# Kernel tuning notes

Hardware: AMD Instinct MI355X
Metric: run time of the kernel (lower is better)

## Reference

```python
import jax, jax.numpy as jnp
import numpy as np

HEADS = 2
BN_EPS = 1e-5


def _upsample2x_bilinear_ac(x):
    # torch nn.Upsample(scale_factor=2, mode='bilinear', align_corners=True)
    B, C, H, W = x.shape

    def grid(n):
        c = jnp.arange(2 * n) * ((n - 1) / (2 * n - 1))  # align_corners mapping
        i0 = jnp.clip(jnp.floor(c).astype(jnp.int32), 0, n - 2)
        w = (c - i0).astype(x.dtype)
        return i0, w

    i0, wh = grid(H)
    j0, ww = grid(W)
    x = x[:, :, i0, :] * (1 - wh)[None, None, :, None] + x[:, :, i0 + 1, :] * wh[None, None, :, None]
    x = x[:, :, :, j0] * (1 - ww) + x[:, :, :, j0 + 1] * ww
    return x


def _self_attn(x, wq, wkv, wo, wob):
    # x: (b, t, d); lucidrains axial_attention SelfAttention
    b, t, d = x.shape
    e = d // HEADS
    q = x @ wq
    k, v = jnp.split(x @ wkv, 2, axis=-1)
    mh = lambda z: z.reshape(b, t, HEADS, e).transpose(0, 2, 1, 3)  # (b,h,t,e)
    q, k, v = mh(q), mh(k), mh(v)
    dots = jnp.einsum('bhie,bhje->bhij', q, k) * (e ** -0.5)
    attn = jax.nn.softmax(dots, axis=-1)
    o = jnp.einsum('bhij,bhje->bhie', attn, v)
    o = o.transpose(0, 2, 1, 3).reshape(b, t, d)
    return o @ wo + wob


def setup_inputs() -> dict:
    key = jax.random.key(0)
    ks = jax.random.split(key, 16)
    C, E = 256, 128
    cat = 2 * C + E
    s = 0.02
    inp = {
        'x': jax.random.normal(ks[0], (4, C, 64, 64), jnp.float32),
        'res': jax.random.normal(ks[1], (4, E, 128, 128), jnp.float32),
        'wq_h': jax.random.normal(ks[2], (C, C), jnp.float32) * s,
        'wkv_h': jax.random.normal(ks[3], (C, 2 * C), jnp.float32) * s,
        'wo_h': jax.random.normal(ks[4], (C, C), jnp.float32) * s,
        'wob_h': jnp.zeros((C,), jnp.float32),
        'wq_w': jax.random.normal(ks[5], (C, C), jnp.float32) * s,
        'wkv_w': jax.random.normal(ks[6], (C, 2 * C), jnp.float32) * s,
        'wo_w': jax.random.normal(ks[7], (C, C), jnp.float32) * s,
        'wob_w': jnp.zeros((C,), jnp.float32),
        'conv_w': jax.random.normal(ks[8], (cat, E), jnp.float32) * s,
        'gamma': jnp.ones((E,), jnp.float32),
        'beta': jnp.zeros((E,), jnp.float32),
    }
    return inp


def reference(x, res, wq_h, wkv_h, wo_h, wob_h, wq_w, wkv_w, wo_w, wob_w, conv_w, gamma, beta):
    xu = _upsample2x_bilinear_ac(x)  # (B,C,2H,2W)
    B, C, H, W = xu.shape
    # axial attention along H (rows): batch over B*W
    ah = xu.transpose(0, 3, 2, 1).reshape(B * W, H, C)
    ah = _self_attn(ah, wq_h, wkv_h, wo_h, wob_h).reshape(B, W, H, C).transpose(0, 3, 2, 1)
    # axial attention along W (cols): batch over B*H
    aw = xu.transpose(0, 2, 3, 1).reshape(B * H, W, C)
    aw = _self_attn(aw, wq_w, wkv_w, wo_w, wob_w).reshape(B, H, W, C).transpose(0, 3, 1, 2)
    x_attn = jax.nn.relu(ah + aw)  # sum_axial_out=True, then ReLU
    cat = jnp.concatenate([x_attn, xu, res], axis=1)  # (B, 2C+E, H, W)
    y = jnp.einsum('bchw,ce->behw', cat, conv_w)  # conv1x1, no bias
    y = jax.nn.relu(y)
    # BatchNorm2d, training-mode batch stats (biased variance)
    mu = y.mean(axis=(0, 2, 3), keepdims=True)
    var = y.var(axis=(0, 2, 3), keepdims=True)
    y = (y - mu) / jnp.sqrt(var + BN_EPS)
    return y * gamma[None, :, None, None] + beta[None, :, None, None]
```

## Files before the change

### kernel.cpp

```cpp
#include <hip/hip_runtime.h>
#include <hip/hip_bf16.h>
#include <cstdio>


typedef short bf16x8 __attribute__((ext_vector_type(8)));
typedef short bf16x4 __attribute__((ext_vector_type(4)));
typedef float f32x4 __attribute__((ext_vector_type(4)));

#define MFMA16(a, b, c) __builtin_amdgcn_mfma_f32_16x16x32_bf16((a), (b), (c), 0, 0, 0)

__device__ __forceinline__ short f2bf(float v) {
  __hip_bfloat16 h = __float2bfloat16(v);
  union { __hip_bfloat16 h; short s; } u; u.h = h; return u.s;
}
__device__ __forceinline__ float bf2f(short s) {
  return __uint_as_float(((unsigned int)(unsigned short)s) << 16);
}
__device__ __forceinline__ int swz(int row, int col) {
  return col ^ ((row & 7) << 3);
}

struct WtAll {
  const float* src[7];
  short* dst[7];
  int K[7], N[7], tile0[7];
};

__global__ __launch_bounds__(256) void k_wt_all(WtAll P) {
  const int bid = blockIdx.x;
  int i = 0;
#pragma unroll
  for (int j = 1; j < 7; j++) if (bid >= P.tile0[j]) i = j;
  const float* src = P.src[i];
  short* dst = P.dst[i];
  const int K = P.K[i], N = P.N[i];
  const int local = bid - P.tile0[i];
  const int ktiles = K >> 5;
  const int nt = local / ktiles, kt = local - nt * ktiles;
  const int k0 = kt * 32, n0 = nt * 32;
  __shared__ float tile[32][33];
  const int tx = threadIdx.x & 31, ty = threadIdx.x >> 5;
#pragma unroll
  for (int r = 0; r < 4; r++)
    tile[ty + r * 8][tx] = src[(size_t)(k0 + ty + r * 8) * N + n0 + tx];
  __syncthreads();
#pragma unroll
  for (int r = 0; r < 4; r++)
    dst[(size_t)(n0 + ty + r * 8) * K + k0 + tx] = f2bf(tile[tx][ty + r * 8]);
}

__global__ __launch_bounds__(256) void k_upsample(const float* __restrict__ x,
                                                  short* __restrict__ xu) {
  __shared__ float ldsV[64][65];
  const int bh = blockIdx.x, z = blockIdx.y;
  const int b = bh >> 7, h = bh & 127;
  const float chf = h * (63.0f / 127.0f);
  int i0 = (int)chf; if (i0 > 62) i0 = 62;
  const float wh = chf - (float)i0;
  const int t = threadIdx.x;
  const int cbase = z * 64;
  const float* xb = x + ((size_t)(b * 256 + cbase) * 64 + i0) * 64;
#pragma unroll
  for (int p = 0; p < 16; p++) {
    const int li = p * 256 + t;
    const int c = li >> 6, w = li & 63;
    const float* px = xb + (size_t)c * 4096 + w;
    const float v0 = px[0], v1 = px[64];
    ldsV[c][w] = v0 * (1.f - wh) + v1 * wh;
  }
  __syncthreads();
  const int cg = t & 7, wi = t >> 3;
  short* xout = xu + (size_t)(bh * 128) * 256 + cbase + cg * 8;
#pragma unroll
  for (int p = 0; p < 4; p++) {
    const int w = p * 32 + wi;
    const float cwf = w * (63.0f / 127.0f);
    int j0 = (int)cwf; if (j0 > 62) j0 = 62;
    const float ww = cwf - (float)j0;
    bf16x8 o;
#pragma unroll
    for (int u = 0; u < 8; u++) {
      const float v0 = ldsV[cg * 8 + u][j0], v1 = ldsV[cg * 8 + u][j0 + 1];
      o[u] = f2bf(v0 * (1.f - ww) + v1 * ww);
    }
    *(bf16x8*)(xout + (size_t)w * 256) = o;
  }
}

__global__ __launch_bounds__(512, 2) void k_fused(const short* __restrict__ xu,
                                                  const short* __restrict__ wqkvT0,
                                                  const short* __restrict__ woT0,
                                                  const float* __restrict__ wob0,
                                                  const float* __restrict__ wob1,
                                                  short* __restrict__ accb0,
                                                  short* __restrict__ accb1) {
  __shared__ __align__(16) short Xs[128][256];
  __shared__ __align__(16) short Qb[128][128];
  __shared__ __align__(16) short Kb[128][128];
  __shared__ __align__(16) short Vtb[128][128];

  const int dir = blockIdx.y;
  const short* wqkvT = wqkvT0 + (size_t)dir * 196608;
  const short* woT   = woT0 + (size_t)dir * 65536;
  const float* wob   = dir ? wob1 : wob0;
  short* accb        = dir ? accb1 : accb0;

  const int s = blockIdx.x;
  const int b = s >> 7, pos = s & 127;
  const int tok0 = b * 16384 + (dir ? pos * 128 : pos);
  const int tstep = dir ? 1 : 128;
  const int tid = threadIdx.x;
  const int lane = tid & 63, wid = tid >> 6;
  const int lr = lane & 15, kb = lane >> 4;
  const int ct = wid * 16;
  const float scale = 0.08838834764831845f;

#pragma unroll
  for (int p = 0; p < 8; p++) {
    const int u = p * 512 + tid;
    const int row = u >> 5, ck = (u & 31) * 8;
    bf16x8 v = *(const bf16x8*)(xu + (size_t)(tok0 + row * tstep) * 256 + ck);
    *(bf16x8*)&Xs[row][swz(row, ck)] = v;
  }

  f32x4 accp[2][8];
#pragma unroll
  for (int i = 0; i < 2; i++)
#pragma unroll
    for (int j = 0; j < 8; j++) accp[i][j] = (f32x4){0.f, 0.f, 0.f, 0.f};

  for (int h = 0; h < 2; h++) {
    const short* wqb = wqkvT + (size_t)(h * 128 + ct + lr) * 256 + kb * 8;
    const short* wkb = wqkvT + (size_t)(256 + h * 128 + ct + lr) * 256 + kb * 8;
    const short* wvb = wqkvT + (size_t)(512 + h * 128 + ct + lr) * 256 + kb * 8;
    bf16x8 wq[8], wk[8], wv[8];
#pragma unroll
    for (int ks = 0; ks < 8; ks++) {
      wq[ks] = *(const bf16x8*)(wqb + ks * 32);
      wk[ks] = *(const bf16x8*)(wkb + ks * 32);
      wv[ks] = *(const bf16x8*)(wvb + ks * 32);
    }

    __syncthreads();

#pragma unroll
    for (int nt = 0; nt < 8; nt++) {
      const int xrow = nt * 16 + lr;
      f32x4 dq = (f32x4){0.f, 0.f, 0.f, 0.f};
      f32x4 dk = (f32x4){0.f, 0.f, 0.f, 0.f};
      f32x4 dv = (f32x4){0.f, 0.f, 0.f, 0.f};
#pragma unroll
      for (int ks = 0; ks < 8; ks++) {
        bf16x8 xf = *(const bf16x8*)&Xs[xrow][swz(xrow, kb * 8 + ks * 32)];
        dq = MFMA16(wq[ks], xf, dq);
        dk = MFMA16(wk[ks], xf, dk);
        dv = MFMA16(xf, wv[ks], dv);
      }
      const int trow = nt * 16 + lr, cc = ct + kb * 4;
      bf16x4 pq = {f2bf(dq[0]), f2bf(dq[1]), f2bf(dq[2]), f2bf(dq[3])};
      bf16x4 pk = {f2bf(dk[0]), f2bf(dk[1]), f2bf(dk[2]), f2bf(dk[3])};
      *(bf16x4*)&Qb[trow][swz(trow, cc)] = pq;
      *(bf16x4*)&Kb[trow][swz(trow, cc)] = pk;
      const int vrow = ct + lr;
      bf16x4 pv = {f2bf(dv[0]), f2bf(dv[1]), f2bf(dv[2]), f2bf(dv[3])};
      *(bf16x4*)&Vtb[vrow][swz(vrow, nt * 16 + kb * 4)] = pv;
    }

    __syncthreads();

    f32x4 s8[8];
#pragma unroll
    for (int i = 0; i < 8; i++) s8[i] = (f32x4){0.f, 0.f, 0.f, 0.f};
    const int qrow = ct + lr;
#pragma unroll
    for (int ks = 0; ks < 4; ks++) {
      bf16x8 aq = *(const bf16x8*)&Qb[qrow][swz(qrow, kb * 8 + ks * 32)];
#pragma unroll
      for (int nj = 0; nj < 8; nj++) {
        const int krow = nj * 16 + lr;
        bf16x8 bk = *(const bf16x8*)&Kb[krow][swz(krow, kb * 8 + ks * 32)];
        s8[nj] = MFMA16(bk, aq, s8[nj]);
      }
    }
    {
      float m = s8[0][0];
#pragma unroll
      for (int nj = 0; nj < 8; nj++)
#pragma unroll
        for (int r = 0; r < 4; r++) m = fmaxf(m, s8[nj][r]);
      m = fmaxf(m, __shfl_xor(m, 16));
      m = fmaxf(m, __shfl_xor(m, 32));
      float sum = 0.f;
#pragma unroll
      for (int nj = 0; nj < 8; nj++)
#pragma unroll
        for (int r = 0; r < 4; r++) {
          s8[nj][r] = __expf((s8[nj][r] - m) * scale);
          sum += s8[nj][r];
        }
      sum += __shfl_xor(sum, 16);
      sum += __shfl_xor(sum, 32);
      const float inv = 1.f / sum;
#pragma unroll
      for (int nj = 0; nj < 8; nj++) {
        bf16x4 pp = {f2bf(s8[nj][0] * inv), f2bf(s8[nj][1] * inv),
                     f2bf(s8[nj][2] * inv), f2bf(s8[nj][3] * inv)};
        *(bf16x4*)&Qb[qrow][swz(qrow, nj * 16 + kb * 4)] = pp;
      }
    }

    f32x4 o8[8];
#pragma unroll
    for (int i = 0; i < 8; i++) o8[i] = (f32x4){0.f, 0.f, 0.f, 0.f};
#pragma unroll
    for (int ks = 0; ks < 4; ks++) {
      bf16x8 bp = *(const bf16x8*)&Qb[qrow][swz(qrow, kb * 8 + ks * 32)];
#pragma unroll
      for (int mi = 0; mi < 8; mi++) {
        const int vrow = mi * 16 + lr;
        bf16x8 av = *(const bf16x8*)&Vtb[vrow][swz(vrow, kb * 8 + ks * 32)];
        o8[mi] = MFMA16(av, bp, o8[mi]);
      }
    }

    __syncthreads();

#pragma unroll
    for (int mi = 0; mi < 8; mi++) {
      const int cc = mi * 16 + kb * 4;
      bf16x4 po = {f2bf(o8[mi][0]), f2bf(o8[mi][1]), f2bf(o8[mi][2]), f2bf(o8[mi][3])};
      *(bf16x4*)&Kb[qrow][swz(qrow, cc)] = po;
    }

    __syncthreads();

    {
      const short* w0 = woT + (size_t)(wid * 32 + lr) * 256 + h * 128 + kb * 8;
      const short* w1 = woT + (size_t)(wid * 32 + 16 + lr) * 256 + h * 128 + kb * 8;
      bf16x8 wa[4], wb2[4];
#pragma unroll
      for (int ks = 0; ks < 4; ks++) {
        wa[ks]  = *(const bf16x8*)(w0 + ks * 32);
        wb2[ks] = *(const bf16x8*)(w1 + ks * 32);
      }
#pragma unroll
      for (int nt = 0; nt < 8; nt++) {
        const int trow = nt * 16 + lr;
#pragma unroll
        for (int ks = 0; ks < 4; ks++) {
          bf16x8 bo = *(const bf16x8*)&Kb[trow][swz(trow, kb * 8 + ks * 32)];
          accp[0][nt] = MFMA16(wa[ks], bo, accp[0][nt]);
          accp[1][nt] = MFMA16(wb2[ks], bo, accp[1][nt]);
        }
      }
    }
  }

#pragma unroll
  for (int mi2 = 0; mi2 < 2; mi2++) {
    const int outc = wid * 32 + mi2 * 16 + kb * 4;
    const float b0 = wob[outc], b1 = wob[outc + 1];
    const float b2 = wob[outc + 2], b3 = wob[outc + 3];
#pragma unroll
    for (int nt = 0; nt < 8; nt++) {
      const int token = tok0 + (nt * 16 + lr) * tstep;
      bf16x4 pv = {f2bf(accp[mi2][nt][0] + b0), f2bf(accp[mi2][nt][1] + b1),
                   f2bf(accp[mi2][nt][2] + b2), f2bf(accp[mi2][nt][3] + b3)};
      *(bf16x4*)(accb + (size_t)token * 256 + outc) = pv;
    }
  }
}

__global__ __launch_bounds__(256) void k_gemm_conv(const short* __restrict__ accb0,
                                                   const short* __restrict__ accb1,
                                                   const short* __restrict__ xu,
                                                   const float* __restrict__ res,
                                                   const short* __restrict__ Bt,
                                                   float* __restrict__ ytmp,
                                                   float* __restrict__ partial) {
  __shared__ float redS[2][128], redS2[2][128];
  const int tid = threadIdx.x;
  const int lane = tid & 63, wid = tid >> 6;
  const int lr = lane & 15, kb = lane >> 4;
  const int wr = wid >> 1, wc = wid & 1;
  const int m0 = blockIdx.y * 128;
  f32x4 acc[4][4];
#pragma unroll
  for (int i = 0; i < 4; i++)
#pragma unroll
    for (int j = 0; j < 4; j++) acc[i][j] = (f32x4){0.f, 0.f, 0.f, 0.f};
  const short* arow0 = accb0 + (size_t)(m0 + wr * 64 + lr) * 256 + kb * 8;
  const short* arow1 = accb1 + (size_t)(m0 + wr * 64 + lr) * 256 + kb * 8;
  const short* arow2 = xu + (size_t)(m0 + wr * 64 + lr) * 256 + kb * 8;
  const short* brow = Bt + (size_t)(wc * 64 + lr) * 640 + kb * 8;
#pragma unroll
  for (int ks = 0; ks < 8; ks++) {
    bf16x8 a[4], b[4];
#pragma unroll
    for (int mi = 0; mi < 4; mi++) {
      bf16x8 t0 = *(const bf16x8*)(arow0 + (size_t)mi * 16 * 256 + ks * 32);
      bf16x8 t1 = *(const bf16x8*)(arow1 + (size_t)mi * 16 * 256 + ks * 32);
      bf16x8 tv;
#pragma unroll
      for (int u = 0; u < 8; u++) {
        float sv = bf2f(t0[u]) + bf2f(t1[u]);
        tv[u] = f2bf(fmaxf(sv, 0.f));
      }
      a[mi] = tv;
    }
#pragma unroll
    for (int nj = 0; nj < 4; nj++)
      b[nj] = *(const bf16x8*)(brow + (size_t)nj * 16 * 640 + ks * 32);
#pragma unroll
    for (int mi = 0; mi < 4; mi++)
#pragma unroll
      for (int nj = 0; nj < 4; nj++)
        acc[mi][nj] = MFMA16(a[mi], b[nj], acc[mi][nj]);
  }
#pragma unroll
  for (int ks = 8; ks < 16; ks++) {
    bf16x8 a[4], b[4];
#pragma unroll
    for (int mi = 0; mi < 4; mi++)
      a[mi] = *(const bf16x8*)(arow2 + (size_t)mi * 16 * 256 + (ks - 8) * 32);
#pragma unroll
    for (int nj = 0; nj < 4; nj++)
      b[nj] = *(const bf16x8*)(brow + (size_t)nj * 16 * 640 + ks * 32);
#pragma unroll
    for (int mi = 0; mi < 4; mi++)
#pragma unroll
      for (int nj = 0; nj < 4; nj++)
        acc[mi][nj] = MFMA16(a[mi], b[nj], acc[mi][nj]);
  }
  const int bC = (m0 >> 14) * 128;
  const int hh = (m0 >> 7) & 127;
#pragma unroll
  for (int ks = 16; ks < 20; ks++) {
    const int e0 = (ks - 16) * 32 + kb * 8;
    bf16x8 a[4], b[4];
#pragma unroll
    for (int mi = 0; mi < 4; mi++) {
      const int wl = wr * 64 + mi * 16 + lr;
      const float* rp = res + ((size_t)(bC + e0) * 128 + hh) * 128 + wl;
      bf16x8 tv;
#pragma unroll
      for (int u = 0; u < 8; u++) tv[u] = f2bf(rp[(size_t)u * 16384]);
      a[mi] = tv;
    }
#pragma unroll
    for (int nj = 0; nj < 4; nj++)
      b[nj] = *(const bf16x8*)(brow + (size_t)nj * 16 * 640 + ks * 32);
#pragma unroll
    for (int mi = 0; mi < 4; mi++)
#pragma unroll
      for (int nj = 0; nj < 4; nj++)
        acc[mi][nj] = MFMA16(a[mi], b[nj], acc[mi][nj]);
  }
#pragma unroll
  for (int nj = 0; nj < 4; nj++) {
    float s = 0.f, s2 = 0.f;
    const int c = wc * 64 + nj * 16 + lr;
#pragma unroll
    for (int mi = 0; mi < 4; mi++) {
      const int rbase = m0 + wr * 64 + mi * 16 + kb * 4;
#pragma unroll
      for (int r = 0; r < 4; r++) {
        const float yv = fmaxf(acc[mi][nj][r], 0.f);
        ytmp[(size_t)(rbase + r) * 128 + c] = yv;
        s += yv; s2 += yv * yv;
      }
    }
    s += __shfl_xor(s, 16);  s += __shfl_xor(s, 32);
    s2 += __shfl_xor(s2, 16); s2 += __shfl_xor(s2, 32);
    if (kb == 0) { redS[wr][c] = s; redS2[wr][c] = s2; }
  }
  __syncthreads();
  if (tid < 128) {
    partial[((size_t)blockIdx.y * 128 + tid) * 2]     = redS[0][tid] + redS[1][tid];
    partial[((size_t)blockIdx.y * 128 + tid) * 2 + 1] = redS2[0][tid] + redS2[1][tid];
  }
}

__global__ __launch_bounds__(128) void k_bnstats2(const float* __restrict__ partial,
                                                  float* __restrict__ stats) {
  const int ch = threadIdx.x;
  float s = 0.f, s2 = 0.f;
  for (int i = 0; i < 512; i++) {
    s  += partial[(size_t)(i * 128 + ch) * 2];
    s2 += partial[(size_t)(i * 128 + ch) * 2 + 1];
  }
  const float mu = s * (1.f / 65536.f);
  const float var = s2 * (1.f / 65536.f) - mu * mu;
  stats[ch * 2] = mu;
  stats[ch * 2 + 1] = rsqrtf(var + 1e-5f);
}

__global__ __launch_bounds__(256) void k_bnout(const float* __restrict__ y,
                                               const float* __restrict__ stats,
                                               const float* __restrict__ gamma,
                                               const float* __restrict__ beta,
                                               float* __restrict__ out) {
  const int bh = blockIdx.x;
  const int b = bh >> 7, h = bh & 127;
  const int w = threadIdx.x & 127, half = threadIdx.x >> 7;
  const float* yp = y + (size_t)(bh * 128 + w) * 128 + half * 64;
  float* op = out + ((size_t)(b * 128) << 14) + h * 128 + w;
#pragma unroll
  for (int e4 = 0; e4 < 16; e4++) {
    f32x4 v = *(const f32x4*)(yp + e4 * 4);
#pragma unroll
    for (int u = 0; u < 4; u++) {
      const int e = half * 64 + e4 * 4 + u;
      const float mu = stats[e * 2], rstd = stats[e * 2 + 1];
      op[(size_t)e << 14] = (v[u] - mu) * rstd * gamma[e] + beta[e];
    }
  }
}

extern "C" void kernel_launch(void* const* d_in, const int* in_sizes, int n_in,
                              void* d_out, int out_size, void* d_ws, size_t ws_size,
                              hipStream_t stream) {
  const float* x      = (const float*)d_in[0];
  const float* res    = (const float*)d_in[1];
  const float* wq_h   = (const float*)d_in[2];
  const float* wkv_h  = (const float*)d_in[3];
  const float* wo_h   = (const float*)d_in[4];
  const float* wob_h  = (const float*)d_in[5];
  const float* wq_w   = (const float*)d_in[6];
  const float* wkv_w  = (const float*)d_in[7];
  const float* wo_w   = (const float*)d_in[8];
  const float* wob_w  = (const float*)d_in[9];
  const float* conv_w = (const float*)d_in[10];
  const float* gamma  = (const float*)d_in[11];
  const float* beta   = (const float*)d_in[12];

  char* ws = (char*)d_ws;
  short* wqkvT[2] = {(short*)(ws + 0), (short*)(ws + 393216)};
  short* woT[2]   = {(short*)(ws + 786432), (short*)(ws + 917504)};
  short* convT    = (short*)(ws + 1048576);
  short* xu       = (short*)(ws + 1245184);
  float* ytmp     = (float*)(ws + 34799616);
  float* partial  = (float*)(ws + 68354048);
  float* stats    = (float*)(ws + 68878336);
  short* accb1    = (short*)(ws + 68879360);
  short* accb0    = (short*)d_out;
  float* out      = (float*)d_out;

  if (ws_size < 102433792ull)
    fprintf(stderr, "kernel_launch: ws_size %zu too small\n", ws_size);

  WtAll P;
  P.src[0] = wq_h;  P.dst[0] = wqkvT[0];          P.K[0] = 256; P.N[0] = 256; P.tile0[0] = 0;
  P.src[1] = wkv_h; P.dst[1] = wqkvT[0] + 65536;  P.K[1] = 256; P.N[1] = 512; P.tile0[1] = 64;
  P.src[2] = wq_w;  P.dst[2] = wqkvT[1];          P.K[2] = 256; P.N[2] = 256; P.tile0[2] = 192;
  P.src[3] = wkv_w; P.dst[3] = wqkvT[1] + 65536;  P.K[3] = 256; P.N[3] = 512; P.tile0[3] = 256;
  P.src[4] = wo_h;  P.dst[4] = woT[0];            P.K[4] = 256; P.N[4] = 256; P.tile0[4] = 384;
  P.src[5] = wo_w;  P.dst[5] = woT[1];            P.K[5] = 256; P.N[5] = 256; P.tile0[5] = 448;
  P.src[6] = conv_w;P.dst[6] = convT;             P.K[6] = 640; P.N[6] = 128; P.tile0[6] = 512;
  k_wt_all<<<592, 256, 0, stream>>>(P);

  k_upsample<<<dim3(512, 4), 256, 0, stream>>>(x, xu);

  k_fused<<<dim3(512, 2), 512, 0, stream>>>(xu, wqkvT[0], woT[0],
                                            wob_h, wob_w, accb0, accb1);

  k_gemm_conv<<<dim3(1, 512), 256, 0, stream>>>(accb0, accb1, xu, res, convT,
                                                ytmp, partial);
  k_bnstats2<<<1, 128, 0, stream>>>(partial, stats);
  k_bnout<<<512, 256, 0, stream>>>(ytmp, stats, gamma, beta, out);
}
```

Measured before the change: 247.9 us.

## Write transposed upsample copy and stream X from global to shrink fused-kernel LDS

The upsample kernel now also writes a W-major transposed copy of the upsampled tensor, so both attention directions read contiguous rows. The fused attention kernel drops its X and V shared-memory tiles, reading X fragments directly from global/L2 and reusing the K buffer for V and the Q buffer for the attention output. Launch bounds rise from 2 to 4 blocks per CU to exploit the smaller LDS footprint. This trades extra global writes and repeated global reads of X, plus extra barriers, for higher occupancy; register pressure under the tighter bound may cause spills.

```diff
diff --git a/kernel.cpp b/kernel.cpp
--- a/kernel.cpp
+++ b/kernel.cpp
@@ -50,7 +50,8 @@
 }
 
 __global__ __launch_bounds__(256) void k_upsample(const float* __restrict__ x,
-                                                  short* __restrict__ xu) {
+                                                  short* __restrict__ xu,
+                                                  short* __restrict__ xuT) {
   __shared__ float ldsV[64][65];
   const int bh = blockIdx.x, z = blockIdx.y;
   const int b = bh >> 7, h = bh & 127;
@@ -71,6 +72,7 @@
   __syncthreads();
   const int cg = t & 7, wi = t >> 3;
   short* xout = xu + (size_t)(bh * 128) * 256 + cbase + cg * 8;
+  short* xoutT = xuT + ((size_t)b * 16384 + h) * 256 + cbase + cg * 8;
 #pragma unroll
   for (int p = 0; p < 4; p++) {
     const int w = p * 32 + wi;
@@ -84,20 +86,20 @@
       o[u] = f2bf(v0 * (1.f - ww) + v1 * ww);
     }
     *(bf16x8*)(xout + (size_t)w * 256) = o;
-  }
-}
-
-__global__ __launch_bounds__(512, 2) void k_fused(const short* __restrict__ xu,
+    *(bf16x8*)(xoutT + (size_t)w * 128 * 256) = o;
+  }
+}
+
+__global__ __launch_bounds__(512, 4) void k_fused(const short* __restrict__ xu,
+                                                  const short* __restrict__ xuT,
                                                   const short* __restrict__ wqkvT0,
                                                   const short* __restrict__ woT0,
                                                   const float* __restrict__ wob0,
                                                   const float* __restrict__ wob1,
                                                   short* __restrict__ accb0,
                                                   short* __restrict__ accb1) {
-  __shared__ __align__(16) short Xs[128][256];
   __shared__ __align__(16) short Qb[128][128];
   __shared__ __align__(16) short Kb[128][128];
-  __shared__ __align__(16) short Vtb[128][128];
 
   const int dir = blockIdx.y;
   const short* wqkvT = wqkvT0 + (size_t)dir * 196608;
@@ -109,20 +111,14 @@
   const int b = s >> 7, pos = s & 127;
   const int tok0 = b * 16384 + (dir ? pos * 128 : pos);
   const int tstep = dir ? 1 : 128;
+  const short* Xb = (dir ? xu : xuT) + ((size_t)b * 16384 + (size_t)pos * 128) * 256;
+
   const int tid = threadIdx.x;
   const int lane = tid & 63, wid = tid >> 6;
   const int lr = lane & 15, kb = lane >> 4;
   const int ct = wid * 16;
   const float scale = 0.08838834764831845f;
 
-#pragma unroll
-  for (int p = 0; p < 8; p++) {
-    const int u = p * 512 + tid;
-    const int row = u >> 5, ck = (u & 31) * 8;
-    bf16x8 v = *(const bf16x8*)(xu + (size_t)(tok0 + row * tstep) * 256 + ck);
-    *(bf16x8*)&Xs[row][swz(row, ck)] = v;
-  }
-
   f32x4 accp[2][8];
 #pragma unroll
   for (int i = 0; i < 2; i++)
@@ -130,42 +126,33 @@
     for (int j = 0; j < 8; j++) accp[i][j] = (f32x4){0.f, 0.f, 0.f, 0.f};
 
   for (int h = 0; h < 2; h++) {
-    const short* wqb = wqkvT + (size_t)(h * 128 + ct + lr) * 256 + kb * 8;
-    const short* wkb = wqkvT + (size_t)(256 + h * 128 + ct + lr) * 256 + kb * 8;
-    const short* wvb = wqkvT + (size_t)(512 + h * 128 + ct + lr) * 256 + kb * 8;
-    bf16x8 wq[8], wk[8], wv[8];
-#pragma unroll
-    for (int ks = 0; ks < 8; ks++) {
-      wq[ks] = *(const bf16x8*)(wqb + ks * 32);
-      wk[ks] = *(const bf16x8*)(wkb + ks * 32);
-      wv[ks] = *(const bf16x8*)(wvb + ks * 32);
-    }
-
-    __syncthreads();
-
-#pragma unroll
-    for (int nt = 0; nt < 8; nt++) {
-      const int xrow = nt * 16 + lr;
-      f32x4 dq = (f32x4){0.f, 0.f, 0.f, 0.f};
-      f32x4 dk = (f32x4){0.f, 0.f, 0.f, 0.f};
-      f32x4 dv = (f32x4){0.f, 0.f, 0.f, 0.f};
+    {
+      const short* wqb = wqkvT + (size_t)(h * 128 + ct + lr) * 256 + kb * 8;
+      const short* wkb = wqkvT + (size_t)(256 + h * 128 + ct + lr) * 256 + kb * 8;
+      bf16x8 wq[8], wk[8];
 #pragma unroll
       for (int ks = 0; ks < 8; ks++) {
-        bf16x8 xf = *(const bf16x8*)&Xs[xrow][swz(xrow, kb * 8 + ks * 32)];
-        dq = MFMA16(wq[ks], xf, dq);
-        dk = MFMA16(wk[ks], xf, dk);
-        dv = MFMA16(xf, wv[ks], dv);
-      }
-      const int trow = nt * 16 + lr, cc = ct + kb * 4;
-      bf16x4 pq = {f2bf(dq[0]), f2bf(dq[1]), f2bf(dq[2]), f2bf(dq[3])};
-      bf16x4 pk = {f2bf(dk[0]), f2bf(dk[1]), f2bf(dk[2]), f2bf(dk[3])};
-      *(bf16x4*)&Qb[trow][swz(trow, cc)] = pq;
-      *(bf16x4*)&Kb[trow][swz(trow, cc)] = pk;
-      const int vrow = ct + lr;
-      bf16x4 pv = {f2bf(dv[0]), f2bf(dv[1]), f2bf(dv[2]), f2bf(dv[3])};
-      *(bf16x4*)&Vtb[vrow][swz(vrow, nt * 16 + kb * 4)] = pv;
-    }
-
+        wq[ks] = *(const bf16x8*)(wqb + ks * 32);
+        wk[ks] = *(const bf16x8*)(wkb + ks * 32);
+      }
+#pragma unroll
+      for (int nt = 0; nt < 8; nt++) {
+        const short* xr = Xb + (size_t)(nt * 16 + lr) * 256 + kb * 8;
+        f32x4 dq = (f32x4){0.f, 0.f, 0.f, 0.f};
+        f32x4 dk = (f32x4){0.f, 0.f, 0.f, 0.f};
+#pragma unroll
+        for (int ks = 0; ks < 8; ks++) {
+          bf16x8 xf = *(const bf16x8*)(xr + ks * 32);
+          dq = MFMA16(wq[ks], xf, dq);
+          dk = MFMA16(wk[ks], xf, dk);
+        }
+        const int trow = nt * 16 + lr, cc = ct + kb * 4;
+        bf16x4 pq = {f2bf(dq[0]), f2bf(dq[1]), f2bf(dq[2]), f2bf(dq[3])};
+        bf16x4 pk = {f2bf(dk[0]), f2bf(dk[1]), f2bf(dk[2]), f2bf(dk[3])};
+        *(bf16x4*)&Qb[trow][swz(trow, cc)] = pq;
+        *(bf16x4*)&Kb[trow][swz(trow, cc)] = pk;
+      }
+    }
     __syncthreads();
 
     f32x4 s8[8];
@@ -208,6 +195,28 @@
         *(bf16x4*)&Qb[qrow][swz(qrow, nj * 16 + kb * 4)] = pp;
       }
     }
+    __syncthreads();
+
+    {
+      const short* wvb = wqkvT + (size_t)(512 + h * 128 + ct + lr) * 256 + kb * 8;
+      bf16x8 wv[8];
+#pragma unroll
+      for (int ks = 0; ks < 8; ks++) wv[ks] = *(const bf16x8*)(wvb + ks * 32);
+#pragma unroll
+      for (int nt = 0; nt < 8; nt++) {
+        const short* xr = Xb + (size_t)(nt * 16 + lr) * 256 + kb * 8;
+        f32x4 dv = (f32x4){0.f, 0.f, 0.f, 0.f};
+#pragma unroll
+        for (int ks = 0; ks < 8; ks++) {
+          bf16x8 xf = *(const bf16x8*)(xr + ks * 32);
+          dv = MFMA16(xf, wv[ks], dv);
+        }
+        const int vrow = ct + lr;
+        bf16x4 pv = {f2bf(dv[0]), f2bf(dv[1]), f2bf(dv[2]), f2bf(dv[3])};
+        *(bf16x4*)&Kb[vrow][swz(vrow, nt * 16 + kb * 4)] = pv;
+      }
+    }
+    __syncthreads();
 
     f32x4 o8[8];
 #pragma unroll
@@ -218,20 +227,16 @@
 #pragma unroll
       for (int mi = 0; mi < 8; mi++) {
         const int vrow = mi * 16 + lr;
-        bf16x8 av = *(const bf16x8*)&Vtb[vrow][swz(vrow, kb * 8 + ks * 32)];
+        bf16x8 av = *(const bf16x8*)&Kb[vrow][swz(vrow, kb * 8 + ks * 32)];
         o8[mi] = MFMA16(av, bp, o8[mi]);
       }
     }
-
-    __syncthreads();
-
 #pragma unroll
     for (int mi = 0; mi < 8; mi++) {
       const int cc = mi * 16 + kb * 4;
       bf16x4 po = {f2bf(o8[mi][0]), f2bf(o8[mi][1]), f2bf(o8[mi][2]), f2bf(o8[mi][3])};
-      *(bf16x4*)&Kb[qrow][swz(qrow, cc)] = po;
-    }
-
+      *(bf16x4*)&Qb[qrow][swz(qrow, cc)] = po;
+    }
     __syncthreads();
 
     {
@@ -248,12 +253,13 @@
         const int trow = nt * 16 + lr;
 #pragma unroll
         for (int ks = 0; ks < 4; ks++) {
-          bf16x8 bo = *(const bf16x8*)&Kb[trow][swz(trow, kb * 8 + ks * 32)];
+          bf16x8 bo = *(const bf16x8*)&Qb[trow][swz(trow, kb * 8 + ks * 32)];
           accp[0][nt] = MFMA16(wa[ks], bo, accp[0][nt]);
           accp[1][nt] = MFMA16(wb2[ks], bo, accp[1][nt]);
         }
       }
     }
+    if (h == 0) __syncthreads();
   }
 
 #pragma unroll
@@ -443,10 +449,11 @@
   float* partial  = (float*)(ws + 68354048);
   float* stats    = (float*)(ws + 68878336);
   short* accb1    = (short*)(ws + 68879360);
+  short* xuT      = (short*)(ws + 102433792);
   short* accb0    = (short*)d_out;
   float* out      = (float*)d_out;
 
-  if (ws_size < 102433792ull)
+  if (ws_size < 135988224ull)
     fprintf(stderr, "kernel_launch: ws_size %zu too small\n", ws_size);
 
   WtAll P;
@@ -459,9 +466,9 @@
   P.src[6] = conv_w;P.dst[6] = convT;             P.K[6] = 640; P.N[6] = 128; P.tile0[6] = 512;
   k_wt_all<<<592, 256, 0, stream>>>(P);
 
-  k_upsample<<<dim3(512, 4), 256, 0, stream>>>(x, xu);
-
-  k_fused<<<dim3(512, 2), 512, 0, stream>>>(xu, wqkvT[0], woT[0],
+  k_upsample<<<dim3(512, 4), 256, 0, stream>>>(x, xu, xuT);
+
+  k_fused<<<dim3(512, 2), 512, 0, stream>>>(xu, xuT, wqkvT[0], woT[0],
                                             wob_h, wob_w, accb0, accb1);
 
   k_gemm_conv<<<dim3(1, 512), 256, 0, stream>>>(accb0, accb1, xu, res, convT,
```

New measurement: 944.7 us. 281% more time.
